# Kernel tuning notes

Hardware: AMD Instinct MI355X
Metric: run time of the kernel (lower is better)

## Reference

```python
import jax, jax.numpy as jnp
import numpy as np

B, L, D, V, K = 4, 2048, 1024, 32, 4096  # batch, seq, embedding_dim, vq_dim, num_embeddings


def setup_inputs() -> dict:
    key = jax.random.key(0)
    k0, k1, k2, k3 = jax.random.split(key, 4)
    h = jax.random.normal(k0, (B, L, D), jnp.float32)
    attn_mask = jnp.ones((B, L), jnp.float32)
    # proj: Linear(D -> V); proj_inv: Linear(V -> D)
    Wp = jax.random.normal(k1, (V, D), jnp.float32) / np.float32(np.sqrt(D))
    bp = jnp.zeros((V,), jnp.float32)
    Wpi = jax.random.normal(k2, (D, V), jnp.float32) / np.float32(np.sqrt(V))
    bpi = jnp.zeros((D,), jnp.float32)
    # embedding init uniform(-1/K, 1/K)
    emb = jax.random.uniform(k3, (K, V), jnp.float32, -1.0 / K, 1.0 / K)
    return {"h": h, "attn_mask": attn_mask, "Wp": Wp, "bp": bp,
            "Wpi": Wpi, "bpi": bpi, "emb": emb}


def reference(h, attn_mask, Wp, bp, Wpi, bpi, emb, temperature=1.0):
    # project + L2 normalize
    hp = jnp.einsum('bld,vd->blv', h, Wp) + bp            # [B,L,V]
    hp = hp / jnp.linalg.norm(hp, axis=-1, keepdims=True)
    # normalize codebook (in torch this is an in-place .data update)
    emb_n = emb / jnp.linalg.norm(emb, axis=-1, keepdims=True)  # [K,V]
    # squared euclidean distances hp vs codebook
    d = (jnp.sum(hp * hp, axis=-1, keepdims=True)
         + jnp.sum(emb_n * emb_n, axis=-1)
         - 2.0 * jnp.einsum('blv,kv->blk', hp, emb_n))    # [B,L,K]
    A = jax.nn.softmax(-d / temperature, axis=-1)         # [B,L,K]
    code = jnp.argmax(A, axis=-1)                         # [B,L]
    h_vq = jnp.einsum('blk,kv->blv', A, emb_n)            # train mode: A @ embedding
    # masked scatter into zeros is equivalent to masking out unselected positions
    m = (attn_mask == 1)
    quantized = jnp.where(m[..., None], h_vq, jnp.float32(0.0))
    vq_code = jnp.where(m, code, 0).astype(jnp.int32)
    quantized = jnp.einsum('blv,dv->bld', quantized, Wpi) + bpi
    vq_loss = jnp.float32(0.0)
    return quantized, vq_code, vq_loss
```

## Files before the change

kernel.cpp:

```cpp
#include <hip/hip_runtime.h>
#include <hip/hip_bf16.h>
#include <math.h>

#define NTOK 8192
#define DIM  1024
#define VDIM 32
#define KCODES 4096

typedef __attribute__((ext_vector_type(8))) short short8;
typedef __attribute__((ext_vector_type(4))) float f32x4;

#define MFMA16(A,B,C) __builtin_amdgcn_mfma_f32_16x16x32_bf16(A, B, C, 0, 0, 0)

__device__ __forceinline__ unsigned short f2bf(float x) {
    unsigned u = __builtin_bit_cast(unsigned, x);
    u += 0x7FFF + ((u >> 16) & 1);
    return (unsigned short)(u >> 16);
}
__device__ __forceinline__ float bf2f(unsigned short b) {
    unsigned u = ((unsigned)b) << 16;
    return __builtin_bit_cast(float, u);
}

struct U4 { unsigned x, y, z, w; };

__device__ __forceinline__ void split8(const float* p, short8* H, short8* L) {
    unsigned hh[4], ll[4];
    #pragma unroll
    for (int i = 0; i < 4; ++i) {
        unsigned short a = f2bf(p[2 * i]);
        unsigned short b = f2bf(p[2 * i + 1]);
        hh[i] = (unsigned)a | ((unsigned)b << 16);
        unsigned short la = f2bf(p[2 * i] - bf2f(a));
        unsigned short lb = f2bf(p[2 * i + 1] - bf2f(b));
        ll[i] = (unsigned)la | ((unsigned)lb << 16);
    }
    U4 uh = {hh[0], hh[1], hh[2], hh[3]};
    U4 ul = {ll[0], ll[1], ll[2], ll[3]};
    *H = __builtin_bit_cast(short8, uh);
    *L = __builtin_bit_cast(short8, ul);
}

#define OFS_E_HI   0
#define OFS_E_LO   131072
#define OFS_ET_HI  262144
#define OFS_ET_LO  393216
#define OFS_WP_HI  524288
#define OFS_WP_LO  557056
#define OFS_WPI_HI 589824
#define OFS_WPI_LO 622592

__global__ __launch_bounds__(256) void k_prep(const float* __restrict__ emb,
                                              const float* __restrict__ Wp,
                                              const float* __restrict__ Wpi,
                                              unsigned short* __restrict__ W,
                                              float* __restrict__ loss_out) {
    __shared__ __align__(16) unsigned short Th[32][72];
    __shared__ __align__(16) unsigned short Tl[32][72];
    int bid = blockIdx.x, tid = threadIdx.x;
    if (bid < 64) {
        int cb = bid * 64;
        int c = tid >> 2, s = tid & 3;
        const float* src = emb + (size_t)(cb + c) * VDIM + s * 8;
        float4 a = *(const float4*)src;
        float4 b = *(const float4*)(src + 4);
        float ps = a.x*a.x + a.y*a.y + a.z*a.z + a.w*a.w
                 + b.x*b.x + b.y*b.y + b.z*b.z + b.w*b.w;
        ps += __shfl_xor(ps, 1);
        ps += __shfl_xor(ps, 2);
        float inv = 1.0f / sqrtf(ps);
        float vals[8] = {a.x*inv, a.y*inv, a.z*inv, a.w*inv,
                         b.x*inv, b.y*inv, b.z*inv, b.w*inv};
        short8 H, L;
        split8(vals, &H, &L);
        *(short8*)(W + OFS_E_HI + (size_t)(cb + c) * VDIM + s * 8) = H;
        *(short8*)(W + OFS_E_LO + (size_t)(cb + c) * VDIM + s * 8) = L;
        #pragma unroll
        for (int j = 0; j < 8; ++j) {
            unsigned short hb = f2bf(vals[j]);
            Th[s * 8 + j][c] = hb;
            Tl[s * 8 + j][c] = f2bf(vals[j] - bf2f(hb));
        }
        __syncthreads();
        int row = tid >> 3, seg = tid & 7;
        *(short8*)(W + OFS_ET_HI + (size_t)row * KCODES + cb + seg * 8) =
            *(const short8*)&Th[row][seg * 8];
        *(short8*)(W + OFS_ET_LO + (size_t)row * KCODES + cb + seg * 8) =
            *(const short8*)&Tl[row][seg * 8];
        if (bid == 0 && tid == 0) loss_out[0] = 0.0f;
    } else if (bid < 80) {
        int i0 = (bid - 64) * 2048 + tid * 8;
        float4 a = *(const float4*)(Wp + i0);
        float4 b = *(const float4*)(Wp + i0 + 4);
        float vals[8] = {a.x, a.y, a.z, a.w, b.x, b.y, b.z, b.w};
        short8 H, L;
        split8(vals, &H, &L);
        *(short8*)(W + OFS_WP_HI + i0) = H;
        *(short8*)(W + OFS_WP_LO + i0) = L;
    } else {
        int i0 = (bid - 80) * 2048 + tid * 8;
        float4 a = *(const float4*)(Wpi + i0);
        float4 b = *(const float4*)(Wpi + i0 + 4);
        float vals[8] = {a.x, a.y, a.z, a.w, b.x, b.y, b.z, b.w};
        short8 H, L;
        split8(vals, &H, &L);
        *(short8*)(W + OFS_WPI_HI + i0) = H;
        *(short8*)(W + OFS_WPI_LO + i0) = L;
    }
}

__global__ __launch_bounds__(1024) void k_fused(const float* __restrict__ h,
                                                const float* __restrict__ mask,
                                                const unsigned short* __restrict__ W,
                                                const float* __restrict__ bp,
                                                const float* __restrict__ bpi,
                                                float* __restrict__ out,
                                                float* __restrict__ code_out) {
    __shared__ __align__(16) float red2[8][32][36];
    __shared__ __align__(16) unsigned short hpB_hi[32][40];
    __shared__ __align__(16) unsigned short hpB_lo[32][40];
    __shared__ __align__(16) unsigned short hvB_hi[32][40];
    __shared__ __align__(16) unsigned short hvB_lo[32][40];
    __shared__ float lred[16][33];
    __shared__ float amred[16][33];
    __shared__ int   aired[16][33];
    __shared__ float invl[32];

    const unsigned short* E_hi   = W + OFS_E_HI;
    const unsigned short* E_lo   = W + OFS_E_LO;
    const unsigned short* Et_hi  = W + OFS_ET_HI;
    const unsigned short* Et_lo  = W + OFS_ET_LO;
    const unsigned short* Wp_hi  = W + OFS_WP_HI;
    const unsigned short* Wp_lo  = W + OFS_WP_LO;
    const unsigned short* Wpi_hi = W + OFS_WPI_HI;
    const unsigned short* Wpi_lo = W + OFS_WPI_LO;

    int tid = threadIdx.x;
    int w = tid >> 6;
    int l = tid & 63;
    int q = l >> 4, m = l & 15;
    int tok0 = blockIdx.x * 32;
    int sig = ((m & 12) << 1) | (m & 3);
    const f32x4 zero4 = {0.f, 0.f, 0.f, 0.f};

    {
        int tt = w >> 3, kw = w & 7;
        f32x4 acc0 = zero4, acc1 = zero4;
        const float* hb = h + (size_t)(tok0 + tt * 16 + m) * DIM + kw * 128 + q * 8;
        const unsigned short* w0h = Wp_hi + (size_t)m * DIM + kw * 128 + q * 8;
        const unsigned short* w0l = Wp_lo + (size_t)m * DIM + kw * 128 + q * 8;
        const unsigned short* w1h = w0h + (size_t)16 * DIM;
        const unsigned short* w1l = w0l + (size_t)16 * DIM;
        #pragma unroll
        for (int c = 0; c < 4; ++c) {
            float4 a = *(const float4*)(hb + c * 32);
            float4 b = *(const float4*)(hb + c * 32 + 4);
            float va[8] = {a.x, a.y, a.z, a.w, b.x, b.y, b.z, b.w};
            short8 Bh, Bl;
            split8(va, &Bh, &Bl);
            short8 A0h = *(const short8*)(w0h + c * 32);
            short8 A0l = *(const short8*)(w0l + c * 32);
            short8 A1h = *(const short8*)(w1h + c * 32);
            short8 A1l = *(const short8*)(w1l + c * 32);
            acc0 = MFMA16(A0l, Bl, acc0); acc0 = MFMA16(A0l, Bh, acc0);
            acc0 = MFMA16(A0h, Bl, acc0); acc0 = MFMA16(A0h, Bh, acc0);
            acc1 = MFMA16(A1l, Bl, acc1); acc1 = MFMA16(A1l, Bh, acc1);
            acc1 = MFMA16(A1h, Bl, acc1); acc1 = MFMA16(A1h, Bh, acc1);
        }
        int slot = tt * 4 + (kw & 3);
        if ((kw & 4) == 0) {
            *(f32x4*)&red2[slot][m][4 * q]      = acc0;
            *(f32x4*)&red2[slot][m][16 + 4 * q] = acc1;
        }
        __syncthreads();
        if (kw & 4) {
            f32x4* d0 = (f32x4*)&red2[slot][m][4 * q];
            f32x4* d1 = (f32x4*)&red2[slot][m][16 + 4 * q];
            *d0 = *d0 + acc0;
            *d1 = *d1 + acc1;
        }
        __syncthreads();
    }
    {
        int t = tid >> 5, v = tid & 31;
        int sb = (t >> 4) * 4, tr = t & 15;
        float s = bp[v];
        #pragma unroll
        for (int j = 0; j < 4; ++j) s += red2[sb + j][tr][v];
        float sq = s * s;
        #pragma unroll
        for (int off = 1; off < 32; off <<= 1) sq += __shfl_xor(sq, off);
        float nv = s * (1.0f / sqrtf(sq));
        unsigned short hb = f2bf(nv);
        hpB_hi[t][v] = hb;
        hpB_lo[t][v] = f2bf(nv - bf2f(hb));
    }
    __syncthreads();

    short8 hp0h = *(const short8*)&hpB_hi[m][q * 8];
    short8 hp0l = *(const short8*)&hpB_lo[m][q * 8];
    short8 hp1h = *(const short8*)&hpB_hi[16 + m][q * 8];
    short8 hp1l = *(const short8*)&hpB_lo[16 + m][q * 8];

    f32x4 hv00 = zero4, hv01 = zero4, hv10 = zero4, hv11 = zero4;
    float ls0 = 0.f, ls1 = 0.f;
    float am0 = -1e30f, am1 = -1e30f;
    int ai0 = 0, ai1 = 0;

    #pragma unroll 1
    for (int c = 0; c < 8; ++c) {
        int cb = w * 256 + c * 32;
        size_t e0 = (size_t)(cb + sig) * VDIM + q * 8;
        short8 E0h = *(const short8*)(E_hi + e0);
        short8 E0l = *(const short8*)(E_lo + e0);
        short8 E1h = *(const short8*)(E_hi + e0 + 4 * VDIM);
        short8 E1l = *(const short8*)(E_lo + e0 + 4 * VDIM);
        size_t t0 = (size_t)sig * KCODES + cb + q * 8;
        short8 T0h = *(const short8*)(Et_hi + t0);
        short8 T0l = *(const short8*)(Et_lo + t0);
        short8 T1h = *(const short8*)(Et_hi + t0 + (size_t)4 * KCODES);
        short8 T1l = *(const short8*)(Et_lo + t0 + (size_t)4 * KCODES);

        {
            f32x4 s0 = MFMA16(E0l, hp0l, zero4);
            s0 = MFMA16(E0l, hp0h, s0);
            s0 = MFMA16(E0h, hp0l, s0);
            s0 = MFMA16(E0h, hp0h, s0);
            f32x4 s1 = MFMA16(E1l, hp0l, zero4);
            s1 = MFMA16(E1l, hp0h, s1);
            s1 = MFMA16(E1h, hp0l, s1);
            s1 = MFMA16(E1h, hp0h, s1);
            float p[8];
            #pragma unroll
            for (int r = 0; r < 4; ++r) {
                float sv = s0[r];
                if (sv > am0) { am0 = sv; ai0 = cb + 8 * q + r; }
                p[r] = __expf(2.0f * sv);
                sv = s1[r];
                if (sv > am0) { am0 = sv; ai0 = cb + 8 * q + 4 + r; }
                p[4 + r] = __expf(2.0f * sv);
            }
            ls0 += ((p[0] + p[1]) + (p[2] + p[3])) + ((p[4] + p[5]) + (p[6] + p[7]));
            short8 Ph, Pl;
            split8(p, &Ph, &Pl);
            hv00 = MFMA16(T0l, Ph, hv00);
            hv00 = MFMA16(T0h, Pl, hv00);
            hv00 = MFMA16(T0h, Ph, hv00);
            hv01 = MFMA16(T1l, Ph, hv01);
            hv01 = MFMA16(T1h, Pl, hv01);
            hv01 = MFMA16(T1h, Ph, hv01);
        }
        {
            f32x4 s0 = MFMA16(E0l, hp1l, zero4);
            s0 = MFMA16(E0l, hp1h, s0);
            s0 = MFMA16(E0h, hp1l, s0);
            s0 = MFMA16(E0h, hp1h, s0);
            f32x4 s1 = MFMA16(E1l, hp1l, zero4);
            s1 = MFMA16(E1l, hp1h, s1);
            s1 = MFMA16(E1h, hp1l, s1);
            s1 = MFMA16(E1h, hp1h, s1);
            float p[8];
            #pragma unroll
            for (int r = 0; r < 4; ++r) {
                float sv = s0[r];
                if (sv > am1) { am1 = sv; ai1 = cb + 8 * q + r; }
                p[r] = __expf(2.0f * sv);
                sv = s1[r];
                if (sv > am1) { am1 = sv; ai1 = cb + 8 * q + 4 + r; }
                p[4 + r] = __expf(2.0f * sv);
            }
            ls1 += ((p[0] + p[1]) + (p[2] + p[3])) + ((p[4] + p[5]) + (p[6] + p[7]));
            short8 Ph, Pl;
            split8(p, &Ph, &Pl);
            hv10 = MFMA16(T0l, Ph, hv10);
            hv10 = MFMA16(T0h, Pl, hv10);
            hv10 = MFMA16(T0h, Ph, hv10);
            hv11 = MFMA16(T1l, Ph, hv11);
            hv11 = MFMA16(T1h, Pl, hv11);
            hv11 = MFMA16(T1h, Ph, hv11);
        }
    }

    #pragma unroll
    for (int off = 16; off <= 32; off <<= 1) {
        ls0 += __shfl_xor(ls0, off);
        ls1 += __shfl_xor(ls1, off);
        float a2 = __shfl_xor(am0, off);
        int   i2 = __shfl_xor(ai0, off);
        if (a2 > am0 || (a2 == am0 && i2 < ai0)) { am0 = a2; ai0 = i2; }
        a2 = __shfl_xor(am1, off);
        i2 = __shfl_xor(ai1, off);
        if (a2 > am1 || (a2 == am1 && i2 < ai1)) { am1 = a2; ai1 = i2; }
    }
    if (q == 0) {
        lred[w][m] = ls0;       amred[w][m] = am0;       aired[w][m] = ai0;
        lred[w][16 + m] = ls1;  amred[w][16 + m] = am1;  aired[w][16 + m] = ai1;
    }
    if (w < 8) {
        *(f32x4*)&red2[w][m][8 * q]          = hv00;
        *(f32x4*)&red2[w][m][8 * q + 4]      = hv01;
        *(f32x4*)&red2[w][16 + m][8 * q]     = hv10;
        *(f32x4*)&red2[w][16 + m][8 * q + 4] = hv11;
    }
    __syncthreads();
    if (w >= 8) {
        f32x4* d;
        d = (f32x4*)&red2[w - 8][m][8 * q];          *d = *d + hv00;
        d = (f32x4*)&red2[w - 8][m][8 * q + 4];      *d = *d + hv01;
        d = (f32x4*)&red2[w - 8][16 + m][8 * q];     *d = *d + hv10;
        d = (f32x4*)&red2[w - 8][16 + m][8 * q + 4]; *d = *d + hv11;
    }
    __syncthreads();
    if (tid < 32) {
        float L = 0.f, A = -1e30f;
        int I = 0x7fffffff;
        #pragma unroll
        for (int ww = 0; ww < 16; ++ww) {
            L += lred[ww][tid];
            float a2 = amred[ww][tid];
            int   i2 = aired[ww][tid];
            if (a2 > A || (a2 == A && i2 < I)) { A = a2; I = i2; }
        }
        bool on = (mask[tok0 + tid] == 1.0f);
        code_out[tok0 + tid] = on ? (float)I : 0.0f;
        invl[tid] = on ? (1.0f / L) : 0.0f;
    }
    __syncthreads();
    {
        int t = tid >> 5, v = tid & 31;
        float x = 0.f;
        #pragma unroll
        for (int s = 0; s < 8; ++s) x += red2[s][t][v];
        x *= invl[t];
        unsigned short hb = f2bf(x);
        hvB_hi[t][v] = hb;
        hvB_lo[t][v] = f2bf(x - bf2f(hb));
    }
    __syncthreads();

    short8 g0h = *(const short8*)&hvB_hi[m][q * 8];
    short8 g0l = *(const short8*)&hvB_lo[m][q * 8];
    short8 g1h = *(const short8*)&hvB_hi[16 + m][q * 8];
    short8 g1l = *(const short8*)&hvB_lo[16 + m][q * 8];
    #pragma unroll
    for (int dt = 0; dt < 4; ++dt) {
        int dbase = w * 64 + dt * 16;
        short8 Ah = *(const short8*)(Wpi_hi + (size_t)(dbase + m) * VDIM + q * 8);
        short8 Al = *(const short8*)(Wpi_lo + (size_t)(dbase + m) * VDIM + q * 8);
        f32x4 o0 = MFMA16(Al, g0h, zero4);
        o0 = MFMA16(Ah, g0l, o0);
        o0 = MFMA16(Ah, g0h, o0);
        f32x4 o1 = MFMA16(Al, g1h, zero4);
        o1 = MFMA16(Ah, g1l, o1);
        o1 = MFMA16(Ah, g1h, o1);
        float4 bias = *(const float4*)(bpi + dbase + 4 * q);
        float4 r0 = make_float4(o0[0] + bias.x, o0[1] + bias.y,
                                o0[2] + bias.z, o0[3] + bias.w);
        float4 r1 = make_float4(o1[0] + bias.x, o1[1] + bias.y,
                                o1[2] + bias.z, o1[3] + bias.w);
        *(float4*)(out + (size_t)(tok0 + m) * DIM + dbase + 4 * q) = r0;
        *(float4*)(out + (size_t)(tok0 + 16 + m) * DIM + dbase + 4 * q) = r1;
    }
}

extern "C" void kernel_launch(void* const* d_in, const int* in_sizes, int n_in,
                              void* d_out, int out_size, void* d_ws, size_t ws_size,
                              hipStream_t stream) {
    const float* h    = (const float*)d_in[0];
    const float* mask = (const float*)d_in[1];
    const float* Wp   = (const float*)d_in[2];
    const float* bp   = (const float*)d_in[3];
    const float* Wpi  = (const float*)d_in[4];
    const float* bpi  = (const float*)d_in[5];
    const float* emb  = (const float*)d_in[6];
    float* out = (float*)d_out;

    unsigned short* W = (unsigned short*)d_ws;
    float* code_out = out + (size_t)NTOK * DIM;
    float* loss_out = code_out + NTOK;

    hipLaunchKernelGGL(k_prep,  dim3(96),  dim3(256),  0, stream, emb, Wp, Wpi, W, loss_out);
    hipLaunchKernelGGL(k_fused, dim3(256), dim3(1024), 0, stream, h, mask, W, bp, bpi, out, code_out);
}
```

Before: 138.4 us.

## Halve tokens per block, prefetch codebook tiles, drop lo term of probabilities

```diff
diff --git a/kernel.cpp b/kernel.cpp
--- a/kernel.cpp
+++ b/kernel.cpp
@@ -39,6 +39,18 @@
     U4 ul = {ll[0], ll[1], ll[2], ll[3]};
     *H = __builtin_bit_cast(short8, uh);
     *L = __builtin_bit_cast(short8, ul);
+}
+
+__device__ __forceinline__ short8 pack8hi(const float* p) {
+    unsigned hh[4];
+    #pragma unroll
+    for (int i = 0; i < 4; ++i) {
+        unsigned short a = f2bf(p[2 * i]);
+        unsigned short b = f2bf(p[2 * i + 1]);
+        hh[i] = (unsigned)a | ((unsigned)b << 16);
+    }
+    U4 uh = {hh[0], hh[1], hh[2], hh[3]};
+    return __builtin_bit_cast(short8, uh);
 }
 
 #define OFS_E_HI   0
@@ -109,22 +121,22 @@
     }
 }
 
-__global__ __launch_bounds__(1024) void k_fused(const float* __restrict__ h,
-                                                const float* __restrict__ mask,
-                                                const unsigned short* __restrict__ W,
-                                                const float* __restrict__ bp,
-                                                const float* __restrict__ bpi,
-                                                float* __restrict__ out,
-                                                float* __restrict__ code_out) {
-    __shared__ __align__(16) float red2[8][32][36];
-    __shared__ __align__(16) unsigned short hpB_hi[32][40];
-    __shared__ __align__(16) unsigned short hpB_lo[32][40];
-    __shared__ __align__(16) unsigned short hvB_hi[32][40];
-    __shared__ __align__(16) unsigned short hvB_lo[32][40];
-    __shared__ float lred[16][33];
-    __shared__ float amred[16][33];
-    __shared__ int   aired[16][33];
-    __shared__ float invl[32];
+__global__ __launch_bounds__(512) void k_fused(const float* __restrict__ h,
+                                               const float* __restrict__ mask,
+                                               const unsigned short* __restrict__ W,
+                                               const float* __restrict__ bp,
+                                               const float* __restrict__ bpi,
+                                               float* __restrict__ out,
+                                               float* __restrict__ code_out) {
+    __shared__ __align__(16) float red2[8][16][36];
+    __shared__ __align__(16) unsigned short hpB_hi[16][40];
+    __shared__ __align__(16) unsigned short hpB_lo[16][40];
+    __shared__ __align__(16) unsigned short hvB_hi[16][40];
+    __shared__ __align__(16) unsigned short hvB_lo[16][40];
+    __shared__ float lred[8][16];
+    __shared__ float amred[8][16];
+    __shared__ int   aired[8][16];
+    __shared__ float invl[16];
 
     const unsigned short* E_hi   = W + OFS_E_HI;
     const unsigned short* E_lo   = W + OFS_E_LO;
@@ -139,16 +151,15 @@
     int w = tid >> 6;
     int l = tid & 63;
     int q = l >> 4, m = l & 15;
-    int tok0 = blockIdx.x * 32;
+    int tok0 = blockIdx.x * 16;
     int sig = ((m & 12) << 1) | (m & 3);
     const f32x4 zero4 = {0.f, 0.f, 0.f, 0.f};
 
     {
-        int tt = w >> 3, kw = w & 7;
         f32x4 acc0 = zero4, acc1 = zero4;
-        const float* hb = h + (size_t)(tok0 + tt * 16 + m) * DIM + kw * 128 + q * 8;
-        const unsigned short* w0h = Wp_hi + (size_t)m * DIM + kw * 128 + q * 8;
-        const unsigned short* w0l = Wp_lo + (size_t)m * DIM + kw * 128 + q * 8;
+        const float* hb = h + (size_t)(tok0 + m) * DIM + w * 128 + q * 8;
+        const unsigned short* w0h = Wp_hi + (size_t)m * DIM + w * 128 + q * 8;
+        const unsigned short* w0l = Wp_lo + (size_t)m * DIM + w * 128 + q * 8;
         const unsigned short* w1h = w0h + (size_t)16 * DIM;
         const unsigned short* w1l = w0l + (size_t)16 * DIM;
         #pragma unroll
@@ -167,26 +178,15 @@
             acc1 = MFMA16(A1l, Bl, acc1); acc1 = MFMA16(A1l, Bh, acc1);
             acc1 = MFMA16(A1h, Bl, acc1); acc1 = MFMA16(A1h, Bh, acc1);
         }
-        int slot = tt * 4 + (kw & 3);
-        if ((kw & 4) == 0) {
-            *(f32x4*)&red2[slot][m][4 * q]      = acc0;
-            *(f32x4*)&red2[slot][m][16 + 4 * q] = acc1;
-        }
-        __syncthreads();
-        if (kw & 4) {
-            f32x4* d0 = (f32x4*)&red2[slot][m][4 * q];
-            f32x4* d1 = (f32x4*)&red2[slot][m][16 + 4 * q];
-            *d0 = *d0 + acc0;
-            *d1 = *d1 + acc1;
-        }
-        __syncthreads();
-    }
+        *(f32x4*)&red2[w][m][4 * q]      = acc0;
+        *(f32x4*)&red2[w][m][16 + 4 * q] = acc1;
+    }
+    __syncthreads();
     {
         int t = tid >> 5, v = tid & 31;
-        int sb = (t >> 4) * 4, tr = t & 15;
         float s = bp[v];
         #pragma unroll
-        for (int j = 0; j < 4; ++j) s += red2[sb + j][tr][v];
+        for (int j = 0; j < 8; ++j) s += red2[j][t][v];
         float sq = s * s;
         #pragma unroll
         for (int off = 1; off < 32; off <<= 1) sq += __shfl_xor(sq, off);
@@ -197,169 +197,129 @@
     }
     __syncthreads();
 
-    short8 hp0h = *(const short8*)&hpB_hi[m][q * 8];
-    short8 hp0l = *(const short8*)&hpB_lo[m][q * 8];
-    short8 hp1h = *(const short8*)&hpB_hi[16 + m][q * 8];
-    short8 hp1l = *(const short8*)&hpB_lo[16 + m][q * 8];
-
-    f32x4 hv00 = zero4, hv01 = zero4, hv10 = zero4, hv11 = zero4;
-    float ls0 = 0.f, ls1 = 0.f;
-    float am0 = -1e30f, am1 = -1e30f;
-    int ai0 = 0, ai1 = 0;
-
-    #pragma unroll 1
-    for (int c = 0; c < 8; ++c) {
-        int cb = w * 256 + c * 32;
-        size_t e0 = (size_t)(cb + sig) * VDIM + q * 8;
-        short8 E0h = *(const short8*)(E_hi + e0);
-        short8 E0l = *(const short8*)(E_lo + e0);
-        short8 E1h = *(const short8*)(E_hi + e0 + 4 * VDIM);
-        short8 E1l = *(const short8*)(E_lo + e0 + 4 * VDIM);
-        size_t t0 = (size_t)sig * KCODES + cb + q * 8;
-        short8 T0h = *(const short8*)(Et_hi + t0);
-        short8 T0l = *(const short8*)(Et_lo + t0);
-        short8 T1h = *(const short8*)(Et_hi + t0 + (size_t)4 * KCODES);
-        short8 T1l = *(const short8*)(Et_lo + t0 + (size_t)4 * KCODES);
-
-        {
-            f32x4 s0 = MFMA16(E0l, hp0l, zero4);
-            s0 = MFMA16(E0l, hp0h, s0);
-            s0 = MFMA16(E0h, hp0l, s0);
-            s0 = MFMA16(E0h, hp0h, s0);
-            f32x4 s1 = MFMA16(E1l, hp0l, zero4);
-            s1 = MFMA16(E1l, hp0h, s1);
-            s1 = MFMA16(E1h, hp0l, s1);
-            s1 = MFMA16(E1h, hp0h, s1);
-            float p[8];
-            #pragma unroll
-            for (int r = 0; r < 4; ++r) {
-                float sv = s0[r];
-                if (sv > am0) { am0 = sv; ai0 = cb + 8 * q + r; }
-                p[r] = __expf(2.0f * sv);
-                sv = s1[r];
-                if (sv > am0) { am0 = sv; ai0 = cb + 8 * q + 4 + r; }
-                p[4 + r] = __expf(2.0f * sv);
-            }
-            ls0 += ((p[0] + p[1]) + (p[2] + p[3])) + ((p[4] + p[5]) + (p[6] + p[7]));
-            short8 Ph, Pl;
-            split8(p, &Ph, &Pl);
-            hv00 = MFMA16(T0l, Ph, hv00);
-            hv00 = MFMA16(T0h, Pl, hv00);
-            hv00 = MFMA16(T0h, Ph, hv00);
-            hv01 = MFMA16(T1l, Ph, hv01);
-            hv01 = MFMA16(T1h, Pl, hv01);
-            hv01 = MFMA16(T1h, Ph, hv01);
+    short8 hph = *(const short8*)&hpB_hi[m][q * 8];
+    short8 hpl = *(const short8*)&hpB_lo[m][q * 8];
+
+    f32x4 hv0 = zero4, hv1 = zero4;
+    float ls = 0.f, am = -1e30f;
+    int ai = 0;
+
+    int cb = w * 512;
+    size_t e0 = (size_t)(cb + sig) * VDIM + q * 8;
+    size_t t0 = (size_t)sig * KCODES + cb + q * 8;
+    short8 E0h = *(const short8*)(E_hi + e0);
+    short8 E0l = *(const short8*)(E_lo + e0);
+    short8 E1h = *(const short8*)(E_hi + e0 + 4 * VDIM);
+    short8 E1l = *(const short8*)(E_lo + e0 + 4 * VDIM);
+    short8 T0h = *(const short8*)(Et_hi + t0);
+    short8 T0l = *(const short8*)(Et_lo + t0);
+    short8 T1h = *(const short8*)(Et_hi + t0 + (size_t)4 * KCODES);
+    short8 T1l = *(const short8*)(Et_lo + t0 + (size_t)4 * KCODES);
+
+    #pragma unroll 2
+    for (int c = 0; c < 16; ++c) {
+        size_t ne = e0 + 1024, nt = t0 + 32;
+        short8 nE0h = *(const short8*)(E_hi + ne);
+        short8 nE0l = *(const short8*)(E_lo + ne);
+        short8 nE1h = *(const short8*)(E_hi + ne + 4 * VDIM);
+        short8 nE1l = *(const short8*)(E_lo + ne + 4 * VDIM);
+        short8 nT0h = *(const short8*)(Et_hi + nt);
+        short8 nT0l = *(const short8*)(Et_lo + nt);
+        short8 nT1h = *(const short8*)(Et_hi + nt + (size_t)4 * KCODES);
+        short8 nT1l = *(const short8*)(Et_lo + nt + (size_t)4 * KCODES);
+
+        f32x4 s0 = MFMA16(E0l, hpl, zero4);
+        s0 = MFMA16(E0l, hph, s0);
+        s0 = MFMA16(E0h, hpl, s0);
+        s0 = MFMA16(E0h, hph, s0);
+        f32x4 s1 = MFMA16(E1l, hpl, zero4);
+        s1 = MFMA16(E1l, hph, s1);
+        s1 = MFMA16(E1h, hpl, s1);
+        s1 = MFMA16(E1h, hph, s1);
+
+        float p[8];
+        int cbase = cb + 8 * q;
+        #pragma unroll
+        for (int r = 0; r < 4; ++r) {
+            float sv = s0[r];
+            if (sv > am) { am = sv; ai = cbase + r; }
+            p[r] = __expf(2.0f * sv);
+            sv = s1[r];
+            if (sv > am) { am = sv; ai = cbase + 4 + r; }
+            p[4 + r] = __expf(2.0f * sv);
         }
-        {
-            f32x4 s0 = MFMA16(E0l, hp1l, zero4);
-            s0 = MFMA16(E0l, hp1h, s0);
-            s0 = MFMA16(E0h, hp1l, s0);
-            s0 = MFMA16(E0h, hp1h, s0);
-            f32x4 s1 = MFMA16(E1l, hp1l, zero4);
-            s1 = MFMA16(E1l, hp1h, s1);
-            s1 = MFMA16(E1h, hp1l, s1);
-            s1 = MFMA16(E1h, hp1h, s1);
-            float p[8];
-            #pragma unroll
-            for (int r = 0; r < 4; ++r) {
-                float sv = s0[r];
-                if (sv > am1) { am1 = sv; ai1 = cb + 8 * q + r; }
-                p[r] = __expf(2.0f * sv);
-                sv = s1[r];
-                if (sv > am1) { am1 = sv; ai1 = cb + 8 * q + 4 + r; }
-                p[4 + r] = __expf(2.0f * sv);
-            }
-            ls1 += ((p[0] + p[1]) + (p[2] + p[3])) + ((p[4] + p[5]) + (p[6] + p[7]));
-            short8 Ph, Pl;
-            split8(p, &Ph, &Pl);
-            hv10 = MFMA16(T0l, Ph, hv10);
-            hv10 = MFMA16(T0h, Pl, hv10);
-            hv10 = MFMA16(T0h, Ph, hv10);
-            hv11 = MFMA16(T1l, Ph, hv11);
-            hv11 = MFMA16(T1h, Pl, hv11);
-            hv11 = MFMA16(T1h, Ph, hv11);
-        }
+        ls += ((p[0] + p[1]) + (p[2] + p[3])) + ((p[4] + p[5]) + (p[6] + p[7]));
+        short8 Ph = pack8hi(p);
+        hv0 = MFMA16(T0l, Ph, hv0);
+        hv0 = MFMA16(T0h, Ph, hv0);
+        hv1 = MFMA16(T1l, Ph, hv1);
+        hv1 = MFMA16(T1h, Ph, hv1);
+
+        E0h = nE0h; E0l = nE0l; E1h = nE1h; E1l = nE1l;
+        T0h = nT0h; T0l = nT0l; T1h = nT1h; T1l = nT1l;
+        e0 = ne; t0 = nt; cb += 32;
     }
 
     #pragma unroll
     for (int off = 16; off <= 32; off <<= 1) {
-        ls0 += __shfl_xor(ls0, off);
-        ls1 += __shfl_xor(ls1, off);
-        float a2 = __shfl_xor(am0, off);
-        int   i2 = __shfl_xor(ai0, off);
-        if (a2 > am0 || (a2 == am0 && i2 < ai0)) { am0 = a2; ai0 = i2; }
-        a2 = __shfl_xor(am1, off);
-        i2 = __shfl_xor(ai1, off);
-        if (a2 > am1 || (a2 == am1 && i2 < ai1)) { am1 = a2; ai1 = i2; }
+        ls += __shfl_xor(ls, off);
+        float a2 = __shfl_xor(am, off);
+        int   i2 = __shfl_xor(ai, off);
+        if (a2 > am || (a2 == am && i2 < ai)) { am = a2; ai = i2; }
     }
     if (q == 0) {
-        lred[w][m] = ls0;       amred[w][m] = am0;       aired[w][m] = ai0;
-        lred[w][16 + m] = ls1;  amred[w][16 + m] = am1;  aired[w][16 + m] = ai1;
-    }
-    if (w < 8) {
-        *(f32x4*)&red2[w][m][8 * q]          = hv00;
-        *(f32x4*)&red2[w][m][8 * q + 4]      = hv01;
-        *(f32x4*)&red2[w][16 + m][8 * q]     = hv10;
-        *(f32x4*)&red2[w][16 + m][8 * q + 4] = hv11;
-    }
-    __syncthreads();
-    if (w >= 8) {
-        f32x4* d;
-        d = (f32x4*)&red2[w - 8][m][8 * q];          *d = *d + hv00;
-        d = (f32x4*)&red2[w - 8][m][8 * q + 4];      *d = *d + hv01;
-        d = (f32x4*)&red2[w - 8][16 + m][8 * q];     *d = *d + hv10;
-        d = (f32x4*)&red2[w - 8][16 + m][8 * q + 4]; *d = *d + hv11;
-    }
-    __syncthreads();
-    if (tid < 32) {
+        lred[w][m] = ls; amred[w][m] = am; aired[w][m] = ai;
+    }
+    *(f32x4*)&red2[w][m][8 * q]     = hv0;
+    *(f32x4*)&red2[w][m][8 * q + 4] = hv1;
+    __syncthreads();
+
+    if (tid < 16) {
         float L = 0.f, A = -1e30f;
         int I = 0x7fffffff;
         #pragma unroll
-        for (int ww = 0; ww < 16; ++ww) {
-            L += lred[ww][tid];
-            float a2 = amred[ww][tid];
-            int   i2 = aired[ww][tid];
+        for (int j = 0; j < 8; ++j) {
+            L += lred[j][tid];
+            float a2 = amred[j][tid];
+            int   i2 = aired[j][tid];
             if (a2 > A || (a2 == A && i2 < I)) { A = a2; I = i2; }
         }
         bool on = (mask[tok0 + tid] == 1.0f);
         code_out[tok0 + tid] = on ? (float)I : 0.0f;
         invl[tid] = on ? (1.0f / L) : 0.0f;
     }
-    __syncthreads();
+    float xsum;
     {
         int t = tid >> 5, v = tid & 31;
         float x = 0.f;
         #pragma unroll
-        for (int s = 0; s < 8; ++s) x += red2[s][t][v];
-        x *= invl[t];
+        for (int j = 0; j < 8; ++j) x += red2[j][t][v];
+        xsum = x;
+    }
+    __syncthreads();
+    {
+        int t = tid >> 5, v = tid & 31;
+        float x = xsum * invl[t];
         unsigned short hb = f2bf(x);
         hvB_hi[t][v] = hb;
         hvB_lo[t][v] = f2bf(x - bf2f(hb));
     }
     __syncthreads();
 
-    short8 g0h = *(const short8*)&hvB_hi[m][q * 8];
-    short8 g0l = *(const short8*)&hvB_lo[m][q * 8];
-    short8 g1h = *(const short8*)&hvB_hi[16 + m][q * 8];
-    short8 g1l = *(const short8*)&hvB_lo[16 + m][q * 8];
+    short8 gh = *(const short8*)&hvB_hi[m][q * 8];
+    short8 gl = *(const short8*)&hvB_lo[m][q * 8];
     #pragma unroll
-    for (int dt = 0; dt < 4; ++dt) {
-        int dbase = w * 64 + dt * 16;
+    for (int dt = 0; dt < 8; ++dt) {
+        int dbase = w * 128 + dt * 16;
         short8 Ah = *(const short8*)(Wpi_hi + (size_t)(dbase + m) * VDIM + q * 8);
         short8 Al = *(const short8*)(Wpi_lo + (size_t)(dbase + m) * VDIM + q * 8);
-        f32x4 o0 = MFMA16(Al, g0h, zero4);
-        o0 = MFMA16(Ah, g0l, o0);
-        o0 = MFMA16(Ah, g0h, o0);
-        f32x4 o1 = MFMA16(Al, g1h, zero4);
-        o1 = MFMA16(Ah, g1l, o1);
-        o1 = MFMA16(Ah, g1h, o1);
+        f32x4 o = MFMA16(Al, gh, zero4);
+        o = MFMA16(Ah, gl, o);
+        o = MFMA16(Ah, gh, o);
         float4 bias = *(const float4*)(bpi + dbase + 4 * q);
-        float4 r0 = make_float4(o0[0] + bias.x, o0[1] + bias.y,
-                                o0[2] + bias.z, o0[3] + bias.w);
-        float4 r1 = make_float4(o1[0] + bias.x, o1[1] + bias.y,
-                                o1[2] + bias.z, o1[3] + bias.w);
+        float4 r0 = make_float4(o[0] + bias.x, o[1] + bias.y,
+                                o[2] + bias.z, o[3] + bias.w);
         *(float4*)(out + (size_t)(tok0 + m) * DIM + dbase + 4 * q) = r0;
-        *(float4*)(out + (size_t)(tok0 + 16 + m) * DIM + dbase + 4 * q) = r1;
     }
 }
 
@@ -379,6 +339,6 @@
     float* code_out = out + (size_t)NTOK * DIM;
     float* loss_out = code_out + NTOK;
 
-    hipLaunchKernelGGL(k_prep,  dim3(96),  dim3(256),  0, stream, emb, Wp, Wpi, W, loss_out);
-    hipLaunchKernelGGL(k_fused, dim3(256), dim3(1024), 0, stream, h, mask, W, bp, bpi, out, code_out);
-}
+    hipLaunchKernelGGL(k_prep,  dim3(96),  dim3(256), 0, stream, emb, Wp, Wpi, W, loss_out);
+    hipLaunchKernelGGL(k_fused, dim3(512), dim3(512), 0, stream, h, mask, W, bp, bpi, out, code_out);
+}
```

After: 155.0 us. +12.0%, slower.
